# Kernel optimization log

Hardware: AMD Instinct MI355X
Metric: run time of the kernel (lower is better)

## Reference

```python
import jax, jax.numpy as jnp
import numpy as np

N_VERTICES = 100000
N_JOINTS = 24
N_BETAS = 300
PARENTS = [0, 0, 0, 0, 1, 2, 3, 4, 5, 6, 7, 8, 9, 9, 9, 12, 13, 14, 16, 17, 18, 19, 20, 21]


def rodrigues(r):
    """r: [N,1,3] axis-angle -> [N,3,3] rotation matrices.

    Original adds N(0,1e-8) noise before the norm purely to avoid 0/0; we use a
    deterministic epsilon inside the sqrt instead (same math up to ~1e-8).
    """
    theta = jnp.sqrt(jnp.sum(r * r, axis=(1, 2), keepdims=True) + 1e-16)  # [N,1,1]
    r_hat = r / theta                                                      # [N,1,3]
    cos = jnp.cos(theta)
    sin = jnp.sin(theta)
    x, y, z = r_hat[:, 0, 0], r_hat[:, 0, 1], r_hat[:, 0, 2]
    zero = jnp.zeros_like(x)
    m = jnp.stack([zero, -z, y, z, zero, -x, -y, x, zero], axis=1).reshape(-1, 3, 3)
    dot = jnp.einsum('nia,nib->nab', r_hat, r_hat)  # outer product r_hat^T r_hat
    eye = jnp.eye(3, dtype=r.dtype)
    return cos * eye + (1.0 - cos) * dot + sin * m


def _with_zeros(R3, t):
    # [3,3],[3] -> [4,4] homogeneous transform
    top = jnp.concatenate([R3, t[:, None]], axis=1)              # [3,4]
    bottom = jnp.array([[0.0, 0.0, 0.0, 1.0]], dtype=R3.dtype)
    return jnp.concatenate([top, bottom], axis=0)


def smpl_forward(beta, pose, v_template, J_regressor, skin_weights, shapedirs, posedirs):
    dtype = v_template.dtype
    # shape blendshapes: [V,3,K] . [K] -> [V,3]
    v_shaped = jnp.einsum('vdk,k->vd', shapedirs, beta) + v_template
    J = J_regressor @ v_shaped                                   # [24,3]

    pose_cube = pose.reshape(-1, 1, 3)                           # [24,1,3]
    R_cube_big = rodrigues(pose_cube)                            # [24,3,3]

    # pose blendshapes
    lrotmin = (R_cube_big[1:] - jnp.eye(3, dtype=dtype)).reshape(-1)   # [207]
    v_posed = v_shaped + jnp.einsum('vdp,p->vd', posedirs, lrotmin)    # [V,3]

    # kinematic chain (fixed 24-step sequential dependency)
    Gs = [_with_zeros(R_cube_big[0], J[0])]
    for i in range(1, N_JOINTS):
        j = PARENTS[i]
        Gs.append(Gs[j] @ _with_zeros(R_cube_big[i], J[i] - J[j]))
    G = jnp.stack(Gs)                                            # [24,4,4]

    # remove rest-pose joint locations: G - pad(G @ [J;0])
    J_h = jnp.concatenate([J, jnp.zeros((N_JOINTS, 1), dtype=dtype)], axis=1)  # [24,4]
    RJ = jnp.einsum('jab,jb->ja', G, J_h)                        # [24,4]
    G = G - jnp.pad(RJ[:, :, None], ((0, 0), (0, 0), (3, 0)))    # subtract into last column

    # linear blend skinning
    T = jnp.einsum('vj,jab->vab', skin_weights, G)               # [V,4,4]
    rest_h = jnp.pad(v_posed, ((0, 0), (0, 1)), constant_values=1.0)  # [V,4]
    v = jnp.einsum('vab,vb->va', T, rest_h)                      # [V,4]
    return v[:, :3]


def setup_inputs() -> dict:
    key = jax.random.key(0)
    ks = jax.random.split(key, 7)
    beta = jax.random.normal(ks[0], (N_BETAS,), dtype=jnp.float32)
    pose = jax.random.normal(ks[1], (N_JOINTS * 3,), dtype=jnp.float32)
    v_template = jax.random.normal(ks[2], (N_VERTICES, 3), dtype=jnp.float32)
    # NonNegUnitSum(axis=1) constraints -> nonnegative rows summing to 1
    Jr = jax.random.uniform(ks[3], (N_JOINTS, N_VERTICES), dtype=jnp.float32)
    J_regressor = Jr / jnp.sum(Jr, axis=1, keepdims=True)
    w = jax.random.uniform(ks[4], (N_VERTICES, N_JOINTS), dtype=jnp.float32)
    skin_weights = w / jnp.sum(w, axis=1, keepdims=True)
    shapedirs = 0.01 * jax.random.normal(ks[5], (N_VERTICES, 3, N_BETAS), dtype=jnp.float32)
    posedirs = 0.01 * jax.random.normal(ks[6], (N_VERTICES, 3, (N_JOINTS - 1) * 9), dtype=jnp.float32)
    return {'beta': beta, 'pose': pose, 'v_template': v_template,
            'J_regressor': J_regressor, 'skin_weights': skin_weights,
            'shapedirs': shapedirs, 'posedirs': posedirs}


def reference(beta, pose, v_template, J_regressor, skin_weights, shapedirs, posedirs):
    return smpl_forward(beta, pose, v_template, J_regressor, skin_weights, shapedirs, posedirs)
```

## Files before the change

### kernel.cpp

```cpp
#include <hip/hip_runtime.h>
#include <math.h>

#define N_V 100000
#define N_J 24
#define N_BETAS 300
#define N_POSE 207
#define NBLKV (N_V / 16)

typedef float f4 __attribute__((ext_vector_type(4)));

__constant__ int c_parents[N_J] = {0,0,0,0,1,2,3,4,5,6,7,8,9,9,9,12,13,14,16,17,18,19,20,21};

__device__ inline void rodrigues9(const float* __restrict__ pose, int j, float R[9]) {
    float x = pose[j*3+0], y = pose[j*3+1], z = pose[j*3+2];
    float th = sqrtf(x*x + y*y + z*z + 1e-16f);
    float inv = 1.0f / th;
    float rx = x*inv, ry = y*inv, rz = z*inv;
    float c = cosf(th), s = sinf(th), o = 1.0f - c;
    R[0] = c + o*rx*rx;      R[1] = o*rx*ry - s*rz;  R[2] = o*rx*rz + s*ry;
    R[3] = o*ry*rx + s*rz;   R[4] = c + o*ry*ry;     R[5] = o*ry*rz - s*rx;
    R[6] = o*rz*rx - s*ry;   R[7] = o*rz*ry + s*rx;  R[8] = c + o*rz*rz;
}

__global__ __launch_bounds__(256) void k_vertex(
        const float* __restrict__ shapedirs, const float* __restrict__ posedirs,
        const float* __restrict__ v_template, const float* __restrict__ beta,
        const float* __restrict__ pose, const float* __restrict__ Jr,
        float* __restrict__ vp, float* __restrict__ jpart) {
    __shared__ float lrot_s[N_POSE];
    __shared__ float vsh[16][3];
    int t = threadIdx.x;
    int lane = t & 63, wave = t >> 6;

    if (t >= 1 && t < N_J) {
        float R[9]; rodrigues9(pose, t, R);
        #pragma unroll
        for (int e = 0; e < 9; ++e)
            lrot_s[(t-1)*9 + e] = R[e] - ((e==0 || e==4 || e==8) ? 1.f : 0.f);
    }
    __syncthreads();

    f4 bv[4];
    #pragma unroll
    for (int it = 0; it < 4; ++it) {
        int i = lane + it * 64;
        int d = (i >= 150) ? 2 : ((i >= 75) ? 1 : 0);
        int k4 = i - d * 75;
        if (it < 3 || i < 225) bv[it] = ((const f4*)beta)[k4];
        else                   bv[it] = (f4){0.f, 0.f, 0.f, 0.f};
    }
    int f0 = 4 * lane;
    f4 lrc0 = { lrot_s[(f0+0)%207], lrot_s[(f0+1)%207], lrot_s[(f0+2)%207], lrot_s[(f0+3)%207] };
    f4 lrc1 = { lrot_s[(f0+256)%207], lrot_s[(f0+257)%207], lrot_s[(f0+258)%207], lrot_s[(f0+259)%207] };
    f4 lrc2 = { lrot_s[(f0+512)%207], lrot_s[(f0+513)%207], lrot_s[(f0+514)%207], lrot_s[(f0+515)%207] };
    float tc = lrot_s[206];

    int vb = blockIdx.x * 16 + wave * 4;

    #pragma unroll 2
    for (int u = 0; u < 4; ++u) {
        int v = vb + u;
        const f4*    sb = (const f4*)(shapedirs + (size_t)v * 900);
        const float* pb = posedirs + (size_t)v * 621;

        f4 s0 = __builtin_nontemporal_load(sb + lane);
        f4 s1 = __builtin_nontemporal_load(sb + lane + 64);
        f4 s2 = __builtin_nontemporal_load(sb + lane + 128);
        f4 s3 = (lane < 33) ? __builtin_nontemporal_load(sb + lane + 192)
                            : (f4){0.f, 0.f, 0.f, 0.f};
        f4 x0, x1, x2 = (f4){0.f, 0.f, 0.f, 0.f};
        __builtin_memcpy(&x0, pb + f0, 16);
        __builtin_memcpy(&x1, pb + f0 + 256, 16);
        if (lane < 27) __builtin_memcpy(&x2, pb + f0 + 512, 16);
        float tail = (lane == 27) ? pb[620] : 0.f;

        float a0 = 0.f, a1 = 0.f, a2 = 0.f;
        float p0 = 0.f, p1 = 0.f, p2 = 0.f;

        float c0 = s0.x*bv[0].x + s0.y*bv[0].y + s0.z*bv[0].z + s0.w*bv[0].w;
        float c1 = s1.x*bv[1].x + s1.y*bv[1].y + s1.z*bv[1].z + s1.w*bv[1].w;
        float c2 = s2.x*bv[2].x + s2.y*bv[2].y + s2.z*bv[2].z + s2.w*bv[2].w;
        float c3 = s3.x*bv[3].x + s3.y*bv[3].y + s3.z*bv[3].z + s3.w*bv[3].w;
        a0 += c0;
        if (lane < 11) a0 += c1; else a1 += c1;
        if (lane < 22) a1 += c2; else a2 += c2;
        a2 += c3;

        float d0 = x0.x*lrc0.x + x0.y*lrc0.y + x0.z*lrc0.z + x0.w*lrc0.w;
        float d1 = x1.x*lrc1.x + x1.y*lrc1.y + x1.z*lrc1.z + x1.w*lrc1.w;
        float d2 = x2.x*lrc2.x + x2.y*lrc2.y + x2.z*lrc2.z + x2.w*lrc2.w;
        if (lane < 51)       p0 += d0;
        else if (lane == 51) { float hi = x0.w * lrc0.w; p0 += d0 - hi; p1 += hi; }
        else                 p1 += d0;
        if (lane < 39)       p1 += d1;
        else if (lane == 39) { float hi = x1.z*lrc1.z + x1.w*lrc1.w; p1 += d1 - hi; p2 += hi; }
        else                 p2 += d1;
        p2 += d2 + tail * tc;

        #pragma unroll
        for (int off = 1; off <= 4; off <<= 1) {
            a0 += __shfl_xor(a0, off); a1 += __shfl_xor(a1, off); a2 += __shfl_xor(a2, off);
            p0 += __shfl_xor(p0, off); p1 += __shfl_xor(p1, off); p2 += __shfl_xor(p2, off);
        }
        int j = lane & 7;
        float val = a0;
        val = (j == 1) ? a1 : val;
        val = (j == 2) ? a2 : val;
        val = (j == 3) ? p0 : val;
        val = (j == 4) ? p1 : val;
        val = (j == 5) ? p2 : val;
        val += __shfl_xor(val, 8);
        val += __shfl_xor(val, 16);
        val += __shfl_xor(val, 32);
        float pj = __shfl(val, lane + 3);

        if (lane < 3) {
            float vsd = val + v_template[(size_t)v*3 + lane];
            vsh[wave*4 + u][lane] = vsd;
            vp[lane * N_V + v] = vsd + pj;
        }
    }
    __syncthreads();

    for (int idx = t; idx < N_J * 16; idx += 256) {
        int j = idx >> 4, vi = idx & 15;
        float w = __builtin_nontemporal_load(Jr + (size_t)j * N_V + blockIdx.x * 16 + vi);
        float s0 = w * vsh[vi][0];
        float s1 = w * vsh[vi][1];
        float s2 = w * vsh[vi][2];
        #pragma unroll
        for (int off = 1; off <= 8; off <<= 1) {
            s0 += __shfl_xor(s0, off); s1 += __shfl_xor(s1, off); s2 += __shfl_xor(s2, off);
        }
        if ((lane & 15) == 0) {
            jpart[(size_t)(j*3+0) * NBLKV + blockIdx.x] = s0;
            jpart[(size_t)(j*3+1) * NBLKV + blockIdx.x] = s1;
            jpart[(size_t)(j*3+2) * NBLKV + blockIdx.x] = s2;
        }
    }
}

__global__ __launch_bounds__(256) void k_jreduce(const float* __restrict__ jpart,
                                                 float* __restrict__ Jg) {
    int c = blockIdx.x;
    const float* col = jpart + (size_t)c * NBLKV;
    int t = threadIdx.x;
    float s = 0.f;
    for (int i = t; i < NBLKV; i += 256) s += col[i];
    #pragma unroll
    for (int off = 32; off; off >>= 1) s += __shfl_xor(s, off);
    __shared__ float red[4];
    int wave = t >> 6, lane = t & 63;
    if (lane == 0) red[wave] = s;
    __syncthreads();
    if (t == 0) Jg[c] = red[0] + red[1] + red[2] + red[3];
}

__global__ __launch_bounds__(256) void k_skin(const float* __restrict__ w,
                                              const float* __restrict__ Jg,
                                              const float* __restrict__ pose,
                                              const float* __restrict__ vp,
                                              float* __restrict__ out) {
    __shared__ float Rsh[N_J][9];
    __shared__ float J[N_J][3];
    __shared__ float G[N_J][16];
    __shared__ float Gp[N_J * 12];
    int t = threadIdx.x;
    if (t < N_J) {
        float R[9]; rodrigues9(pose, t, R);
        #pragma unroll
        for (int e = 0; e < 9; ++e) Rsh[t][e] = R[e];
    }
    if (t < N_J * 3) J[t/3][t%3] = Jg[t];
    __syncthreads();
    if (t < 16) {
        int a = t / 4, b = t % 4;
        float g;
        if (a < 3) g = (b < 3) ? Rsh[0][a*3 + b] : J[0][a];
        else       g = (b == 3) ? 1.f : 0.f;
        G[0][t] = g;
    }
    __syncthreads();
    for (int i = 1; i < N_J; ++i) {
        int p = c_parents[i];
        if (t < 16) {
            int a = t / 4, b = t % 4;
            float acc = 0.f;
            #pragma unroll
            for (int k = 0; k < 4; ++k) {
                float Ak;
                if (k < 3) Ak = (b < 3) ? Rsh[i][k*3 + b] : (J[i][k] - J[p][k]);
                else       Ak = (b == 3) ? 1.f : 0.f;
                acc += G[p][a*4 + k] * Ak;
            }
            G[i][t] = acc;
        }
        __syncthreads();
    }
    for (int i = t; i < N_J * 12; i += 256) {
        int j = i / 12, r = i % 12, a = r / 4, b = r % 4;
        float g = G[j][a*4 + b];
        if (b == 3)
            g -= G[j][a*4+0]*J[j][0] + G[j][a*4+1]*J[j][1] + G[j][a*4+2]*J[j][2];
        Gp[i] = g;
    }
    __syncthreads();

    int v = blockIdx.x * 256 + t;
    if (v >= N_V) return;
    float T[12];
    #pragma unroll
    for (int r = 0; r < 12; ++r) T[r] = 0.f;
    const f4* wv = (const f4*)(w + (size_t)v * 24);
    #pragma unroll
    for (int q = 0; q < 6; ++q) {
        f4 ww = __builtin_nontemporal_load(wv + q);
        float wj[4] = {ww.x, ww.y, ww.z, ww.w};
        #pragma unroll
        for (int jj = 0; jj < 4; ++jj) {
            const float* g = &Gp[(q*4 + jj) * 12];
            #pragma unroll
            for (int r = 0; r < 12; ++r) T[r] += wj[jj] * g[r];
        }
    }
    float px = vp[v], py = vp[N_V + v], pz = vp[2*N_V + v];
    out[v*3+0] = T[0]*px + T[1]*py + T[2]*pz  + T[3];
    out[v*3+1] = T[4]*px + T[5]*py + T[6]*pz  + T[7];
    out[v*3+2] = T[8]*px + T[9]*py + T[10]*pz + T[11];
}

extern "C" void kernel_launch(void* const* d_in, const int* in_sizes, int n_in,
                              void* d_out, int out_size, void* d_ws, size_t ws_size,
                              hipStream_t stream) {
    const float* beta       = (const float*)d_in[0];
    const float* pose       = (const float*)d_in[1];
    const float* v_template = (const float*)d_in[2];
    const float* Jr         = (const float*)d_in[3];
    const float* skin_w     = (const float*)d_in[4];
    const float* shapedirs  = (const float*)d_in[5];
    const float* posedirs   = (const float*)d_in[6];
    float* out = (float*)d_out;

    float* ws    = (float*)d_ws;
    float* ws_vp = ws;
    float* ws_jp = ws + 3*N_V;
    float* ws_J  = ws + 3*N_V + 72*NBLKV;

    k_vertex<<<NBLKV, 256, 0, stream>>>(shapedirs, posedirs, v_template,
                                        beta, pose, Jr, ws_vp, ws_jp);
    k_jreduce<<<N_J * 3, 256, 0, stream>>>(ws_jp, ws_J);
    k_skin<<<(N_V + 255) / 256, 256, 0, stream>>>(skin_w, ws_J, pose, ws_vp, out);
}
```

Baseline: 127.3 us.

## Fuse vertex, joint-reduce and skinning kernels into one cooperative persistent kernel

The three separate launches are merged into one persistent cooperative kernel sized from occupancy, with grid.sync() separating the vertex/blendshape phase, the joint-regressor reduction and the skinning phase. Each block now accumulates its joint partial sums in shared memory across all the vertex groups it handles, so far fewer partials are written and reduced. This removes launch gaps and shrinks the jpart traffic, at the cost of grid-wide barrier overhead, a redundant kinematic-chain computation per persistent block, and a grid-stride skin loop. It also relies on cooperative launch support and on the 256-CU assumption in NCU.

```diff
diff --git a/kernel.cpp b/kernel.cpp
--- a/kernel.cpp
+++ b/kernel.cpp
@@ -1,11 +1,14 @@
 #include <hip/hip_runtime.h>
+#include <hip/hip_cooperative_groups.h>
 #include <math.h>
+
+namespace cg = cooperative_groups;
 
 #define N_V 100000
 #define N_J 24
-#define N_BETAS 300
 #define N_POSE 207
-#define NBLKV (N_V / 16)
+#define NGRP 6250
+#define NCU 256
 
 typedef float f4 __attribute__((ext_vector_type(4)));
 
@@ -22,16 +25,28 @@
     R[6] = o*rz*rx - s*ry;   R[7] = o*rz*ry + s*rx;  R[8] = c + o*rz*rz;
 }
 
-__global__ __launch_bounds__(256) void k_vertex(
+__global__ __launch_bounds__(256, 3) void k_fused(
         const float* __restrict__ shapedirs, const float* __restrict__ posedirs,
         const float* __restrict__ v_template, const float* __restrict__ beta,
         const float* __restrict__ pose, const float* __restrict__ Jr,
-        float* __restrict__ vp, float* __restrict__ jpart) {
+        const float* __restrict__ skw,
+        float* __restrict__ vp, float* __restrict__ jpart,
+        float* __restrict__ Jg, float* __restrict__ out) {
+    cg::grid_group grid = cg::this_grid();
+
     __shared__ float lrot_s[N_POSE];
     __shared__ float vsh[16][3];
+    __shared__ float jacc[N_J * 3];
+    __shared__ float red[4];
+    __shared__ float Rsh[N_J][9];
+    __shared__ float J[N_J][3];
+    __shared__ float G[N_J][16];
+    __shared__ float Gp[N_J * 12];
+
     int t = threadIdx.x;
     int lane = t & 63, wave = t >> 6;
 
+    for (int i = t; i < N_J * 3; i += 256) jacc[i] = 0.f;
     if (t >= 1 && t < N_J) {
         float R[9]; rodrigues9(pose, t, R);
         #pragma unroll
@@ -55,117 +70,109 @@
     f4 lrc2 = { lrot_s[(f0+512)%207], lrot_s[(f0+513)%207], lrot_s[(f0+514)%207], lrot_s[(f0+515)%207] };
     float tc = lrot_s[206];
 
-    int vb = blockIdx.x * 16 + wave * 4;
-
-    #pragma unroll 2
-    for (int u = 0; u < 4; ++u) {
-        int v = vb + u;
-        const f4*    sb = (const f4*)(shapedirs + (size_t)v * 900);
-        const float* pb = posedirs + (size_t)v * 621;
-
-        f4 s0 = __builtin_nontemporal_load(sb + lane);
-        f4 s1 = __builtin_nontemporal_load(sb + lane + 64);
-        f4 s2 = __builtin_nontemporal_load(sb + lane + 128);
-        f4 s3 = (lane < 33) ? __builtin_nontemporal_load(sb + lane + 192)
-                            : (f4){0.f, 0.f, 0.f, 0.f};
-        f4 x0, x1, x2 = (f4){0.f, 0.f, 0.f, 0.f};
-        __builtin_memcpy(&x0, pb + f0, 16);
-        __builtin_memcpy(&x1, pb + f0 + 256, 16);
-        if (lane < 27) __builtin_memcpy(&x2, pb + f0 + 512, 16);
-        float tail = (lane == 27) ? pb[620] : 0.f;
-
-        float a0 = 0.f, a1 = 0.f, a2 = 0.f;
-        float p0 = 0.f, p1 = 0.f, p2 = 0.f;
-
-        float c0 = s0.x*bv[0].x + s0.y*bv[0].y + s0.z*bv[0].z + s0.w*bv[0].w;
-        float c1 = s1.x*bv[1].x + s1.y*bv[1].y + s1.z*bv[1].z + s1.w*bv[1].w;
-        float c2 = s2.x*bv[2].x + s2.y*bv[2].y + s2.z*bv[2].z + s2.w*bv[2].w;
-        float c3 = s3.x*bv[3].x + s3.y*bv[3].y + s3.z*bv[3].z + s3.w*bv[3].w;
-        a0 += c0;
-        if (lane < 11) a0 += c1; else a1 += c1;
-        if (lane < 22) a1 += c2; else a2 += c2;
-        a2 += c3;
-
-        float d0 = x0.x*lrc0.x + x0.y*lrc0.y + x0.z*lrc0.z + x0.w*lrc0.w;
-        float d1 = x1.x*lrc1.x + x1.y*lrc1.y + x1.z*lrc1.z + x1.w*lrc1.w;
-        float d2 = x2.x*lrc2.x + x2.y*lrc2.y + x2.z*lrc2.z + x2.w*lrc2.w;
-        if (lane < 51)       p0 += d0;
-        else if (lane == 51) { float hi = x0.w * lrc0.w; p0 += d0 - hi; p1 += hi; }
-        else                 p1 += d0;
-        if (lane < 39)       p1 += d1;
-        else if (lane == 39) { float hi = x1.z*lrc1.z + x1.w*lrc1.w; p1 += d1 - hi; p2 += hi; }
-        else                 p2 += d1;
-        p2 += d2 + tail * tc;
-
-        #pragma unroll
-        for (int off = 1; off <= 4; off <<= 1) {
-            a0 += __shfl_xor(a0, off); a1 += __shfl_xor(a1, off); a2 += __shfl_xor(a2, off);
-            p0 += __shfl_xor(p0, off); p1 += __shfl_xor(p1, off); p2 += __shfl_xor(p2, off);
-        }
-        int j = lane & 7;
-        float val = a0;
-        val = (j == 1) ? a1 : val;
-        val = (j == 2) ? a2 : val;
-        val = (j == 3) ? p0 : val;
-        val = (j == 4) ? p1 : val;
-        val = (j == 5) ? p2 : val;
-        val += __shfl_xor(val, 8);
-        val += __shfl_xor(val, 16);
-        val += __shfl_xor(val, 32);
-        float pj = __shfl(val, lane + 3);
-
-        if (lane < 3) {
-            float vsd = val + v_template[(size_t)v*3 + lane];
-            vsh[wave*4 + u][lane] = vsd;
-            vp[lane * N_V + v] = vsd + pj;
-        }
-    }
-    __syncthreads();
-
-    for (int idx = t; idx < N_J * 16; idx += 256) {
-        int j = idx >> 4, vi = idx & 15;
-        float w = __builtin_nontemporal_load(Jr + (size_t)j * N_V + blockIdx.x * 16 + vi);
-        float s0 = w * vsh[vi][0];
-        float s1 = w * vsh[vi][1];
-        float s2 = w * vsh[vi][2];
-        #pragma unroll
-        for (int off = 1; off <= 8; off <<= 1) {
-            s0 += __shfl_xor(s0, off); s1 += __shfl_xor(s1, off); s2 += __shfl_xor(s2, off);
-        }
-        if ((lane & 15) == 0) {
-            jpart[(size_t)(j*3+0) * NBLKV + blockIdx.x] = s0;
-            jpart[(size_t)(j*3+1) * NBLKV + blockIdx.x] = s1;
-            jpart[(size_t)(j*3+2) * NBLKV + blockIdx.x] = s2;
-        }
-    }
-}
-
-__global__ __launch_bounds__(256) void k_jreduce(const float* __restrict__ jpart,
-                                                 float* __restrict__ Jg) {
-    int c = blockIdx.x;
-    const float* col = jpart + (size_t)c * NBLKV;
-    int t = threadIdx.x;
-    float s = 0.f;
-    for (int i = t; i < NBLKV; i += 256) s += col[i];
-    #pragma unroll
-    for (int off = 32; off; off >>= 1) s += __shfl_xor(s, off);
-    __shared__ float red[4];
-    int wave = t >> 6, lane = t & 63;
-    if (lane == 0) red[wave] = s;
-    __syncthreads();
-    if (t == 0) Jg[c] = red[0] + red[1] + red[2] + red[3];
-}
-
-__global__ __launch_bounds__(256) void k_skin(const float* __restrict__ w,
-                                              const float* __restrict__ Jg,
-                                              const float* __restrict__ pose,
-                                              const float* __restrict__ vp,
-                                              float* __restrict__ out) {
-    __shared__ float Rsh[N_J][9];
-    __shared__ float J[N_J][3];
-    __shared__ float G[N_J][16];
-    __shared__ float Gp[N_J * 12];
-    int t = threadIdx.x;
+    for (int g = blockIdx.x; g < NGRP; g += gridDim.x) {
+        int vb = g * 16 + wave * 4;
+        #pragma unroll 2
+        for (int u = 0; u < 4; ++u) {
+            int v = vb + u;
+            const f4*    sb = (const f4*)(shapedirs + (size_t)v * 900);
+            const float* pb = posedirs + (size_t)v * 621;
+
+            f4 s0 = __builtin_nontemporal_load(sb + lane);
+            f4 s1 = __builtin_nontemporal_load(sb + lane + 64);
+            f4 s2 = __builtin_nontemporal_load(sb + lane + 128);
+            f4 s3 = (lane < 33) ? __builtin_nontemporal_load(sb + lane + 192)
+                                : (f4){0.f, 0.f, 0.f, 0.f};
+            f4 x0, x1, x2 = (f4){0.f, 0.f, 0.f, 0.f};
+            __builtin_memcpy(&x0, pb + f0, 16);
+            __builtin_memcpy(&x1, pb + f0 + 256, 16);
+            if (lane < 27) __builtin_memcpy(&x2, pb + f0 + 512, 16);
+            float tail = (lane == 27) ? pb[620] : 0.f;
+
+            float a0 = 0.f, a1 = 0.f, a2 = 0.f;
+            float p0 = 0.f, p1 = 0.f, p2 = 0.f;
+
+            float c0 = s0.x*bv[0].x + s0.y*bv[0].y + s0.z*bv[0].z + s0.w*bv[0].w;
+            float c1 = s1.x*bv[1].x + s1.y*bv[1].y + s1.z*bv[1].z + s1.w*bv[1].w;
+            float c2 = s2.x*bv[2].x + s2.y*bv[2].y + s2.z*bv[2].z + s2.w*bv[2].w;
+            float c3 = s3.x*bv[3].x + s3.y*bv[3].y + s3.z*bv[3].z + s3.w*bv[3].w;
+            a0 += c0;
+            if (lane < 11) a0 += c1; else a1 += c1;
+            if (lane < 22) a1 += c2; else a2 += c2;
+            a2 += c3;
+
+            float d0 = x0.x*lrc0.x + x0.y*lrc0.y + x0.z*lrc0.z + x0.w*lrc0.w;
+            float d1 = x1.x*lrc1.x + x1.y*lrc1.y + x1.z*lrc1.z + x1.w*lrc1.w;
+            float d2 = x2.x*lrc2.x + x2.y*lrc2.y + x2.z*lrc2.z + x2.w*lrc2.w;
+            if (lane < 51)       p0 += d0;
+            else if (lane == 51) { float hi = x0.w * lrc0.w; p0 += d0 - hi; p1 += hi; }
+            else                 p1 += d0;
+            if (lane < 39)       p1 += d1;
+            else if (lane == 39) { float hi = x1.z*lrc1.z + x1.w*lrc1.w; p1 += d1 - hi; p2 += hi; }
+            else                 p2 += d1;
+            p2 += d2 + tail * tc;
+
+            #pragma unroll
+            for (int off = 1; off <= 4; off <<= 1) {
+                a0 += __shfl_xor(a0, off); a1 += __shfl_xor(a1, off); a2 += __shfl_xor(a2, off);
+                p0 += __shfl_xor(p0, off); p1 += __shfl_xor(p1, off); p2 += __shfl_xor(p2, off);
+            }
+            int jj = lane & 7;
+            float val = a0;
+            val = (jj == 1) ? a1 : val;
+            val = (jj == 2) ? a2 : val;
+            val = (jj == 3) ? p0 : val;
+            val = (jj == 4) ? p1 : val;
+            val = (jj == 5) ? p2 : val;
+            val += __shfl_xor(val, 8);
+            val += __shfl_xor(val, 16);
+            val += __shfl_xor(val, 32);
+            float pj = __shfl(val, lane + 3);
+
+            if (lane < 3) {
+                float vsd = val + v_template[(size_t)v*3 + lane];
+                vsh[wave*4 + u][lane] = vsd;
+                vp[lane * N_V + v] = vsd + pj;
+            }
+        }
+        __syncthreads();
+        #pragma unroll
+        for (int pass = 0; pass < 2; ++pass) {
+            int idx = t + pass * 256;
+            if (idx < N_J * 16) {
+                int j = idx >> 4, vi = idx & 15;
+                float w = __builtin_nontemporal_load(Jr + (size_t)j * N_V + g * 16 + vi);
+                float s0 = w * vsh[vi][0];
+                float s1 = w * vsh[vi][1];
+                float s2 = w * vsh[vi][2];
+                #pragma unroll
+                for (int off = 1; off <= 8; off <<= 1) {
+                    s0 += __shfl_xor(s0, off); s1 += __shfl_xor(s1, off); s2 += __shfl_xor(s2, off);
+                }
+                if ((lane & 15) == 0) {
+                    jacc[j*3+0] += s0; jacc[j*3+1] += s1; jacc[j*3+2] += s2;
+                }
+            }
+        }
+        __syncthreads();
+    }
+    if (t < N_J * 3) jpart[(size_t)blockIdx.x * (N_J*3) + t] = jacc[t];
+
+    grid.sync();
+
+    for (int c = blockIdx.x; c < N_J * 3; c += gridDim.x) {
+        float s = 0.f;
+        for (int i = t; i < (int)gridDim.x; i += 256) s += jpart[(size_t)i * (N_J*3) + c];
+        #pragma unroll
+        for (int off = 32; off; off >>= 1) s += __shfl_xor(s, off);
+        if (lane == 0) red[wave] = s;
+        __syncthreads();
+        if (t == 0) Jg[c] = red[0] + red[1] + red[2] + red[3];
+        __syncthreads();
+    }
+
+    grid.sync();
+
     if (t < N_J) {
         float R[9]; rodrigues9(pose, t, R);
         #pragma unroll
@@ -206,27 +213,31 @@
     }
     __syncthreads();
 
-    int v = blockIdx.x * 256 + t;
-    if (v >= N_V) return;
-    float T[12];
-    #pragma unroll
-    for (int r = 0; r < 12; ++r) T[r] = 0.f;
-    const f4* wv = (const f4*)(w + (size_t)v * 24);
-    #pragma unroll
-    for (int q = 0; q < 6; ++q) {
-        f4 ww = __builtin_nontemporal_load(wv + q);
-        float wj[4] = {ww.x, ww.y, ww.z, ww.w};
-        #pragma unroll
-        for (int jj = 0; jj < 4; ++jj) {
-            const float* g = &Gp[(q*4 + jj) * 12];
-            #pragma unroll
-            for (int r = 0; r < 12; ++r) T[r] += wj[jj] * g[r];
-        }
-    }
-    float px = vp[v], py = vp[N_V + v], pz = vp[2*N_V + v];
-    out[v*3+0] = T[0]*px + T[1]*py + T[2]*pz  + T[3];
-    out[v*3+1] = T[4]*px + T[5]*py + T[6]*pz  + T[7];
-    out[v*3+2] = T[8]*px + T[9]*py + T[10]*pz + T[11];
+    const int NVB = (N_V + 255) / 256;
+    for (int vb3 = blockIdx.x; vb3 < NVB; vb3 += gridDim.x) {
+        int v = vb3 * 256 + t;
+        if (v < N_V) {
+            float T[12];
+            #pragma unroll
+            for (int r = 0; r < 12; ++r) T[r] = 0.f;
+            const f4* wv = (const f4*)(skw + (size_t)v * 24);
+            #pragma unroll
+            for (int q = 0; q < 6; ++q) {
+                f4 ww = __builtin_nontemporal_load(wv + q);
+                float wj[4] = {ww.x, ww.y, ww.z, ww.w};
+                #pragma unroll
+                for (int jj = 0; jj < 4; ++jj) {
+                    const float* g = &Gp[(q*4 + jj) * 12];
+                    #pragma unroll
+                    for (int r = 0; r < 12; ++r) T[r] += wj[jj] * g[r];
+                }
+            }
+            float px = vp[v], py = vp[N_V + v], pz = vp[2*N_V + v];
+            out[v*3+0] = T[0]*px + T[1]*py + T[2]*pz  + T[3];
+            out[v*3+1] = T[4]*px + T[5]*py + T[6]*pz  + T[7];
+            out[v*3+2] = T[8]*px + T[9]*py + T[10]*pz + T[11];
+        }
+    }
 }
 
 extern "C" void kernel_launch(void* const* d_in, const int* in_sizes, int n_in,
@@ -242,12 +253,20 @@
     float* out = (float*)d_out;
 
     float* ws    = (float*)d_ws;
-    float* ws_vp = ws;
-    float* ws_jp = ws + 3*N_V;
-    float* ws_J  = ws + 3*N_V + 72*NBLKV;
-
-    k_vertex<<<NBLKV, 256, 0, stream>>>(shapedirs, posedirs, v_template,
-                                        beta, pose, Jr, ws_vp, ws_jp);
-    k_jreduce<<<N_J * 3, 256, 0, stream>>>(ws_jp, ws_J);
-    k_skin<<<(N_V + 255) / 256, 256, 0, stream>>>(skin_w, ws_J, pose, ws_vp, out);
+    float* vp    = ws;
+    float* jpart = ws + 3*N_V;
+    float* Jg    = ws + 3*N_V + 2048*72;
+
+    int nb = 0;
+    hipOccupancyMaxActiveBlocksPerMultiprocessor(&nb, k_fused, 256, 0);
+    if (nb < 1) nb = 1;
+    if (nb > 8) nb = 8;
+    int grid = nb * NCU;
+    if (grid > NGRP) grid = NGRP;
+
+    void* args[] = { (void*)&shapedirs, (void*)&posedirs, (void*)&v_template,
+                     (void*)&beta, (void*)&pose, (void*)&Jr, (void*)&skin_w,
+                     (void*)&vp, (void*)&jpart, (void*)&Jg, (void*)&out };
+    hipLaunchCooperativeKernel((void*)k_fused, dim3(grid), dim3(256),
+                               args, 0, stream);
 }
```

Measured after the change: 324.9 us. 155% more time.
